# Kernel tuning notes

Measured on AMD Instinct MI355X. Metric: run time of the kernel, lower is better.

Reference implementation:

```python
import jax, jax.numpy as jnp
import numpy as np

C = 512
CQK = C // 8

def setup_inputs() -> dict:
    key = jax.random.key(0)
    ks = jax.random.split(key, 9)
    B, L = 8, 2048
    s = 0.02
    return {
        "x": jax.random.normal(ks[0], (B, C, L), jnp.float32),
        "Wq": jax.random.normal(ks[1], (CQK, C), jnp.float32) * s,
        "bq": jax.random.normal(ks[2], (CQK,), jnp.float32) * s,
        "Wk": jax.random.normal(ks[3], (CQK, C), jnp.float32) * s,
        "bk": jax.random.normal(ks[4], (CQK,), jnp.float32) * s,
        "Wv": jax.random.normal(ks[5], (C, C), jnp.float32) * s,
        "bv": jax.random.normal(ks[6], (C,), jnp.float32) * s,
        "Wo": jax.random.normal(ks[7], (C, C), jnp.float32) * s,
        "bo": jax.random.normal(ks[8], (C,), jnp.float32) * s,
    }

def reference(x, Wq, bq, Wk, bk, Wv, bv, Wo, bo):
    # x: [B, C, L]; 1x1 Conv1d == per-position linear over channels
    scale = CQK ** -0.5
    q = jnp.einsum('oc,bcl->bol', Wq, x) + bq[None, :, None]   # [B, CQK, L]
    k = jnp.einsum('oc,bcl->bol', Wk, x) + bk[None, :, None]   # [B, CQK, L]
    v = jnp.einsum('oc,bcl->bol', Wv, x) + bv[None, :, None]   # [B, C, L]
    scores = jnp.einsum('bcq,bck->bqk', q, k) * scale          # [B, L, L]
    attn = jax.nn.softmax(scores, axis=-1)
    out = jnp.einsum('bqk,bck->bcq', attn, v)                  # [B, C, L]
    out = jnp.einsum('oc,bcl->bol', Wo, out) + bo[None, :, None]
    return out + x
```

## Files before the change

kernel.cpp:

```cpp
#include <hip/hip_runtime.h>
#include <hip/hip_bf16.h>

typedef __hip_bfloat16 bf16;
using bf16x8 = __attribute__((ext_vector_type(8))) short;
using f32x4  = __attribute__((ext_vector_type(4))) float;

#define C_DIM 512
#define L_DIM 2048
#define B_DIM 8

#define MFMA16(a, b, c) __builtin_amdgcn_mfma_f32_16x16x32_bf16(a, b, c, 0, 0, 0)

__device__ __forceinline__ float fast_exp2(float x) {
#if __has_builtin(__builtin_amdgcn_exp2f)
    return __builtin_amdgcn_exp2f(x);
#else
    return exp2f(x);
#endif
}

static const size_t OFF_XT  = 0;
static const size_t OFF_WQB = 16777216;
static const size_t OFF_WKB = 16842752;
static const size_t OFF_WVB = 16908288;
static const size_t OFF_WOB = 17432576;
static const size_t OFF_QT  = 17956864;
static const size_t OFF_KT  = 20054016;
static const size_t OFF_VT  = 22151168;
static const size_t OFF_O1  = 38928384;

__global__ void k_wcvt(const float* __restrict__ Wq, const float* __restrict__ Wk,
                       const float* __restrict__ Wv, const float* __restrict__ Wo,
                       bf16* __restrict__ Wqb, bf16* __restrict__ Wkb,
                       bf16* __restrict__ Wvb, bf16* __restrict__ Wob) {
    int i = (blockIdx.x * 256 + threadIdx.x) * 2;
    const float* s;
    bf16* dst;
    if (i < 32768)       { s = Wq + i;            dst = Wqb + i; }
    else if (i < 65536)  { s = Wk + (i - 32768);  dst = Wkb + (i - 32768); }
    else if (i < 327680) { s = Wv + (i - 65536);  dst = Wvb + (i - 65536); }
    else                 { s = Wo + (i - 327680); dst = Wob + (i - 327680); }
    float2 v = *reinterpret_cast<const float2*>(s);
    *reinterpret_cast<__hip_bfloat162*>(dst) = __float22bfloat162_rn(make_float2(v.x, v.y));
}

__global__ __launch_bounds__(256) void k_tr(const float* __restrict__ x,
                                            bf16* __restrict__ xT) {
    __shared__ float T[64][65];
    const int b = blockIdx.z;
    const int l0 = blockIdx.x * 64, c0 = blockIdx.y * 64;
    const int tx = threadIdx.x & 63, ty = threadIdx.x >> 6;

    const float* xp = x + ((size_t)b * C_DIM + c0) * L_DIM + l0;
#pragma unroll
    for (int i = 0; i < 16; ++i) {
        int c = i * 4 + ty;
        T[c][tx] = xp[(size_t)c * L_DIM + tx];
    }
    __syncthreads();
    const int c2 = (threadIdx.x & 31) * 2;
    const int lr = threadIdx.x >> 5;
#pragma unroll
    for (int i = 0; i < 8; ++i) {
        int l = i * 8 + lr;
        __hip_bfloat162 u = __float22bfloat162_rn(make_float2(T[c2][l], T[c2 + 1][l]));
        *reinterpret_cast<__hip_bfloat162*>(
            &xT[((size_t)b * L_DIM + l0 + l) * C_DIM + c0 + c2]) = u;
    }
}

__global__ __launch_bounds__(256, 2) void k_qkv(const bf16* __restrict__ xT,
                                                const bf16* __restrict__ Wqb, const float* __restrict__ bq,
                                                const bf16* __restrict__ Wkb, const float* __restrict__ bk,
                                                const bf16* __restrict__ Wvb, const float* __restrict__ bv,
                                                bf16* __restrict__ qT, bf16* __restrict__ kT,
                                                bf16* __restrict__ vTT) {
    const int b = blockIdx.z, y = blockIdx.y, bx = blockIdx.x;
    const int tid = threadIdx.x;
    const int w = tid >> 6, lane = tid & 63, quad = lane >> 4, l15 = lane & 15;
    const int wm = w >> 1, wn = w & 1;
    const size_t bL = (size_t)b * L_DIM;

    __shared__ __align__(16) char lds[32768];

    const bf16* Aptr;
    const bf16* Bptr;
    if (y == 0) {
        Aptr = xT + (bL + bx * 128) * C_DIM;
        Bptr = Wqb;
    } else {
        Aptr = Wvb + (size_t)((y - 1) * 128) * C_DIM;
        Bptr = xT + (bL + bx * 128) * C_DIM;
    }

    f32x4 acc[4][4];
#pragma unroll
    for (int i = 0; i < 4; ++i)
#pragma unroll
        for (int j = 0; j < 4; ++j) acc[i][j] = (f32x4){0.f, 0.f, 0.f, 0.f};

    const int srow = tid >> 2;
    const int schk = tid & 3;
    auto stage = [&](int kt, int d) __attribute__((always_inline)) {
#pragma unroll
        for (int j = 0; j < 2; ++j) {
            const int row = j * 64 + srow;
            const int sg = schk ^ ((row >> 1) & 3);
            const bf16* sa = Aptr + (size_t)row * C_DIM + kt * 32 + sg * 8;
            __builtin_amdgcn_global_load_lds(
                (const __attribute__((address_space(1))) void*)sa,
                (__attribute__((address_space(3))) void*)(lds + d * 8192 + j * 4096 + w * 1024),
                16, 0, 0);
        }
#pragma unroll
        for (int j = 0; j < 2; ++j) {
            const int row = j * 64 + srow;
            const int sg = schk ^ ((row >> 1) & 3);
            const bf16* sb = Bptr + (size_t)row * C_DIM + kt * 32 + sg * 8;
            __builtin_amdgcn_global_load_lds(
                (const __attribute__((address_space(1))) void*)sb,
                (__attribute__((address_space(3))) void*)(lds + 16384 + d * 8192 + j * 4096 + w * 1024),
                16, 0, 0);
        }
    };

    const int fsw = (quad ^ ((l15 >> 1) & 3)) << 4;

    stage(0, 0);
    asm volatile("s_waitcnt vmcnt(0)" ::: "memory");
    __builtin_amdgcn_s_barrier();
    __builtin_amdgcn_sched_barrier(0);

    for (int kt = 0; kt < 16; ++kt) {
        const int d = kt & 1;
        if (kt < 15) stage(kt + 1, d ^ 1);

        char* Ab = lds + d * 8192;
        char* Bb = lds + 16384 + d * 8192;
        bf16x8 af[4], bfr[4];
#pragma unroll
        for (int mi = 0; mi < 4; ++mi)
            af[mi] = *(const bf16x8*)(Ab + (wm * 64 + mi * 16 + l15) * 64 + fsw);
#pragma unroll
        for (int ni = 0; ni < 4; ++ni)
            bfr[ni] = *(const bf16x8*)(Bb + (wn * 64 + ni * 16 + l15) * 64 + fsw);

#pragma unroll
        for (int mi = 0; mi < 4; ++mi)
#pragma unroll
            for (int ni = 0; ni < 4; ++ni)
                acc[mi][ni] = MFMA16(af[mi], bfr[ni], acc[mi][ni]);

        if (kt < 15) {
            asm volatile("s_waitcnt vmcnt(0)" ::: "memory");
            __builtin_amdgcn_s_barrier();
            __builtin_amdgcn_sched_barrier(0);
        }
    }

    if (y == 0) {
        const int mbase = bx * 128 + wm * 64;
        const float* bias = wn ? bk : bq;
        bf16* dst = wn ? kT : qT;
        const float sc = wn ? 1.0f : 0.18033688f;
        float bb[4];
#pragma unroll
        for (int ni = 0; ni < 4; ++ni) bb[ni] = bias[ni * 16 + l15];
#pragma unroll
        for (int mi = 0; mi < 4; ++mi)
#pragma unroll
            for (int r = 0; r < 4; ++r) {
                int l = mbase + mi * 16 + quad * 4 + r;
#pragma unroll
                for (int ni = 0; ni < 4; ++ni)
                    dst[(bL + l) * 64 + ni * 16 + l15] = __float2bfloat16((acc[mi][ni][r] + bb[ni]) * sc);
            }
    } else {
        const int cbase = (y - 1) * 128 + wm * 64;
        const int lbase = bx * 128 + wn * 64;
#pragma unroll
        for (int mi = 0; mi < 4; ++mi)
#pragma unroll
            for (int r = 0; r < 4; ++r) {
                int c = cbase + mi * 16 + quad * 4 + r;
                float bb = bv[c];
#pragma unroll
                for (int ni = 0; ni < 4; ++ni)
                    vTT[((size_t)b * C_DIM + c) * L_DIM + lbase + ni * 16 + l15] =
                        __float2bfloat16(acc[mi][ni][r] + bb);
            }
    }
}

__global__ __launch_bounds__(512, 4) void k_attn(const bf16* __restrict__ qT,
                                                 const bf16* __restrict__ kT,
                                                 const bf16* __restrict__ vTT,
                                                 bf16* __restrict__ o1) {
    const int bid = blockIdx.x;
    const int b  = bid & 7;
    const int qt = (bid >> 3) & 15;
    const int cs = bid >> 7;
    const int q0 = qt * 128;
    const int c0 = cs * 128;
    const int tid = threadIdx.x;
    const int w = tid >> 6, lane = tid & 63;
    const int quad = lane >> 4, l15 = lane & 15;

    __shared__ __align__(16) char lds[49152];

    const size_t bL = (size_t)b * L_DIM;
    const bf16* kb = kT + bL * 64;

    bf16x8 qf0, qf1;
    {
        const bf16* qrow = qT + (bL + q0 + w * 16 + l15) * 64;
        qf0 = *(const bf16x8*)(qrow + quad * 8);
        qf1 = *(const bf16x8*)(qrow + 32 + quad * 8);
    }

    f32x4 acc[8];
#pragma unroll
    for (int cg = 0; cg < 8; ++cg) acc[cg] = (f32x4){0.f, 0.f, 0.f, 0.f};
    f32x4 sacc = (f32x4){0.f, 0.f, 0.f, 0.f};

    bf16x8 onesB;
#pragma unroll
    for (int j = 0; j < 8; ++j) onesB[j] = (short)0x3F80;

    const int vbase = l15 * 64 + ((quad ^ ((l15 >> 1) & 3)) << 4);
    const int srcA  = ((quad & 1) * 32 + l15) * 4;

    auto stage = [&](int kt, int bufi) __attribute__((always_inline)) {
        {
            const int cl = tid >> 2, ps = tid & 3;
            const int pg = ps ^ ((cl >> 1) & 3);
            const bf16* src = vTT + ((size_t)b * C_DIM + c0 + cl) * L_DIM + kt * 32 + pg * 8;
            __builtin_amdgcn_global_load_lds(
                (const __attribute__((address_space(1))) void*)src,
                (__attribute__((address_space(3))) void*)(lds + bufi * 8192 + w * 1024),
                16, 0, 0);
        }
        {
            const int i = tid & 255, k = i >> 3, sl = i & 7;
            const int sg = sl ^ (k & 7);
            const bf16* src = kb + (size_t)(kt * 32 + k) * 64 + sg * 8;
            __builtin_amdgcn_global_load_lds(
                (const __attribute__((address_space(1))) void*)src,
                (__attribute__((address_space(3))) void*)(lds + 32768 + bufi * 4096 + (w & 3) * 1024),
                16, 0, 0);
        }
    };

    auto exppack = [&](const f32x4& s, unsigned& lo, unsigned& hi)
        __attribute__((always_inline)) {
        float p0 = fast_exp2(s[0] - 5.7707801f);
        float p1 = fast_exp2(s[1] - 5.7707801f);
        float p2 = fast_exp2(s[2] - 5.7707801f);
        float p3 = fast_exp2(s[3] - 5.7707801f);
        __hip_bfloat162 h01 = __float22bfloat162_rn(make_float2(p0, p1));
        __hip_bfloat162 h23 = __float22bfloat162_rn(make_float2(p2, p3));
        lo = *reinterpret_cast<unsigned*>(&h01);
        hi = *reinterpret_cast<unsigned*>(&h23);
    };

    bf16x8 paA, paB;

    auto step = [&](int i, bf16x8& paC, bf16x8& paN,
                    bool doPV, bool doStage, int vm) __attribute__((always_inline)) -> void {
        bf16x8 vBr[8];
        if (doPV) {
            char* Vb = lds + ((i - 1) & 3) * 8192;
#pragma unroll
            for (int cg = 0; cg < 8; ++cg)
                vBr[cg] = *(const bf16x8*)(Vb + vbase + cg * 1024);
        }
        if (vm == 0) asm volatile("s_waitcnt vmcnt(0)" ::: "memory");
        else         asm volatile("s_waitcnt vmcnt(2)" ::: "memory");
        __builtin_amdgcn_s_barrier();
        __builtin_amdgcn_sched_barrier(0);
        if (doStage) stage(i + 2, (i + 2) & 3);

        char* Kb = lds + 32768 + (i & 3) * 4096;
        bf16x8 kf[2][2];
#pragma unroll
        for (int kh = 0; kh < 2; ++kh)
#pragma unroll
            for (int h2 = 0; h2 < 2; ++h2)
                kf[kh][h2] = *(const bf16x8*)(Kb + (kh * 16 + l15) * 128 +
                                              (((h2 * 4 + quad) ^ (l15 & 7)) << 4));

        unsigned hh[2][2];
#pragma unroll
        for (int kh = 0; kh < 2; ++kh) {
            f32x4 s = {0.f, 0.f, 0.f, 0.f};
            s = MFMA16(kf[kh][0], qf0, s);
            s = MFMA16(kf[kh][1], qf1, s);
            exppack(s, hh[kh][0], hh[kh][1]);
        }

        if (doPV) {
#pragma unroll
            for (int cg = 0; cg < 8; ++cg)
                acc[cg] = MFMA16(paC, vBr[cg], acc[cg]);
            sacc = MFMA16(paC, onesB, sacc);
        }

        {
            int sel01 = (quad < 2) ? (int)hh[0][0] : (int)hh[1][0];
            int sel23 = (quad < 2) ? (int)hh[0][1] : (int)hh[1][1];
            int a0 = __builtin_amdgcn_ds_bpermute(srcA,      sel01);
            int a1 = __builtin_amdgcn_ds_bpermute(srcA,      sel23);
            int a2 = __builtin_amdgcn_ds_bpermute(srcA + 64, sel01);
            int a3 = __builtin_amdgcn_ds_bpermute(srcA + 64, sel23);
            int4 pi = make_int4(a0, a1, a2, a3);
            paN = *reinterpret_cast<bf16x8*>(&pi);
        }
    };

    stage(0, 0);
    stage(1, 1);
    step(0, paA, paA, false, true, 2);
    for (int i = 1; i < 63; i += 2) {
        step(i,     paA, paB, true, true,        2);
        step(i + 1, paB, paA, true, (i + 1) <= 61, 2);
    }
    step(63, paA, paB, true, false, 0);

    {
        char* Vb = lds + 3 * 8192;
#pragma unroll
        for (int cg = 0; cg < 8; ++cg) {
            bf16x8 vB = *(const bf16x8*)(Vb + vbase + cg * 1024);
            acc[cg] = MFMA16(paB, vB, acc[cg]);
        }
        sacc = MFMA16(paB, onesB, sacc);
    }

#pragma unroll
    for (int r = 0; r < 4; ++r) {
        float iv = 1.f / sacc[r];
        const size_t base = (bL + q0 + w * 16 + quad * 4 + r) * C_DIM + c0;
#pragma unroll
        for (int cg = 0; cg < 8; ++cg)
            o1[base + cg * 16 + l15] = __float2bfloat16(acc[cg][r] * iv);
    }
}

__global__ __launch_bounds__(256, 2) void k_out(const float* __restrict__ x,
                                                const bf16* __restrict__ Wob,
                                                const float* __restrict__ bo,
                                                const bf16* __restrict__ o1,
                                                float* __restrict__ out) {
    const int b = blockIdx.z;
    const int tid = threadIdx.x;
    const int w = tid >> 6, lane = tid & 63, quad = lane >> 4, l15 = lane & 15;
    const int wm = w >> 1, wn = w & 1;
    const int mbase = blockIdx.y * 128 + wm * 64;
    const int nbase = blockIdx.x * 128 + wn * 64;
    const size_t bL = (size_t)b * L_DIM;

    f32x4 acc[4][4];
#pragma unroll
    for (int i = 0; i < 4; ++i)
#pragma unroll
        for (int j = 0; j < 4; ++j) acc[i][j] = (f32x4){0.f, 0.f, 0.f, 0.f};

    const bf16* arow[4];
    const bf16* brow[4];
#pragma unroll
    for (int mi = 0; mi < 4; ++mi) arow[mi] = Wob + (size_t)(mbase + mi * 16 + l15) * C_DIM;
#pragma unroll
    for (int ni = 0; ni < 4; ++ni) brow[ni] = o1 + (bL + nbase + ni * 16 + l15) * C_DIM;

    bf16x8 af[4], bfr[4], afn[4], bfn[4];
    {
        const int ko = quad * 8;
#pragma unroll
        for (int mi = 0; mi < 4; ++mi) af[mi] = *(const bf16x8*)(arow[mi] + ko);
#pragma unroll
        for (int ni = 0; ni < 4; ++ni) bfr[ni] = *(const bf16x8*)(brow[ni] + ko);
    }
    for (int kt = 0; kt < 16; ++kt) {
        if (kt < 15) {
            const int ko = (kt + 1) * 32 + quad * 8;
#pragma unroll
            for (int mi = 0; mi < 4; ++mi) afn[mi] = *(const bf16x8*)(arow[mi] + ko);
#pragma unroll
            for (int ni = 0; ni < 4; ++ni) bfn[ni] = *(const bf16x8*)(brow[ni] + ko);
        }
#pragma unroll
        for (int mi = 0; mi < 4; ++mi)
#pragma unroll
            for (int ni = 0; ni < 4; ++ni)
                acc[mi][ni] = MFMA16(af[mi], bfr[ni], acc[mi][ni]);
#pragma unroll
        for (int i = 0; i < 4; ++i) { af[i] = afn[i]; bfr[i] = bfn[i]; }
    }

#pragma unroll
    for (int mi = 0; mi < 4; ++mi)
#pragma unroll
        for (int r = 0; r < 4; ++r) {
            int row = mbase + mi * 16 + quad * 4 + r;
            float bb = bo[row];
            size_t base = ((size_t)b * C_DIM + row) * L_DIM + nbase;
#pragma unroll
            for (int ni = 0; ni < 4; ++ni) {
                size_t idx = base + ni * 16 + l15;
                out[idx] = acc[mi][ni][r] + bb + x[idx];
            }
        }
}

extern "C" void kernel_launch(void* const* d_in, const int* in_sizes, int n_in,
                              void* d_out, int out_size, void* d_ws, size_t ws_size,
                              hipStream_t stream) {
    const float* x  = (const float*)d_in[0];
    const float* Wq = (const float*)d_in[1];
    const float* bq = (const float*)d_in[2];
    const float* Wk = (const float*)d_in[3];
    const float* bk = (const float*)d_in[4];
    const float* Wv = (const float*)d_in[5];
    const float* bv = (const float*)d_in[6];
    const float* Wo = (const float*)d_in[7];
    const float* bo = (const float*)d_in[8];

    char* wsb = (char*)d_ws;
    bf16* xT  = (bf16*)(wsb + OFF_XT);
    bf16* Wqb = (bf16*)(wsb + OFF_WQB);
    bf16* Wkb = (bf16*)(wsb + OFF_WKB);
    bf16* Wvb = (bf16*)(wsb + OFF_WVB);
    bf16* Wob = (bf16*)(wsb + OFF_WOB);
    bf16* qT  = (bf16*)(wsb + OFF_QT);
    bf16* kT  = (bf16*)(wsb + OFF_KT);
    bf16* vTT = (bf16*)(wsb + OFF_VT);
    bf16* o1  = (bf16*)(wsb + OFF_O1);
    float* out = (float*)d_out;

    k_wcvt<<<dim3(1152), 256, 0, stream>>>(Wq, Wk, Wv, Wo, Wqb, Wkb, Wvb, Wob);
    k_tr<<<dim3(L_DIM / 64, C_DIM / 64, B_DIM), 256, 0, stream>>>(x, xT);
    k_qkv<<<dim3(16, 5, B_DIM), 256, 0, stream>>>(xT, Wqb, bq, Wkb, bk, Wvb, bv, qT, kT, vTT);
    k_attn<<<dim3(512), 512, 0, stream>>>(qT, kT, vTT, o1);
    k_out<<<dim3(16, 4, B_DIM), 256, 0, stream>>>(x, Wob, bo, o1, out);
}
```

Baseline: 143.4 us.

## Stage k_out GEMM operands through swizzled LDS with direct global-to-LDS loads

```diff
diff --git a/kernel.cpp b/kernel.cpp
--- a/kernel.cpp
+++ b/kernel.cpp
@@ -355,48 +355,80 @@
     const int tid = threadIdx.x;
     const int w = tid >> 6, lane = tid & 63, quad = lane >> 4, l15 = lane & 15;
     const int wm = w >> 1, wn = w & 1;
+    const size_t bL = (size_t)b * L_DIM;
+
+    __shared__ __align__(16) char lds[32768];
+
+    const bf16* Aptr = Wob + (size_t)(blockIdx.y * 128) * C_DIM;
+    const bf16* Bptr = o1 + (bL + blockIdx.x * 128) * C_DIM;
+
+    f32x4 acc[4][4];
+#pragma unroll
+    for (int i = 0; i < 4; ++i)
+#pragma unroll
+        for (int j = 0; j < 4; ++j) acc[i][j] = (f32x4){0.f, 0.f, 0.f, 0.f};
+
+    const int srow = tid >> 2;
+    const int schk = tid & 3;
+    auto stage = [&](int kt, int d) __attribute__((always_inline)) {
+#pragma unroll
+        for (int j = 0; j < 2; ++j) {
+            const int row = j * 64 + srow;
+            const int sg = schk ^ ((row >> 1) & 3);
+            const bf16* sa = Aptr + (size_t)row * C_DIM + kt * 32 + sg * 8;
+            __builtin_amdgcn_global_load_lds(
+                (const __attribute__((address_space(1))) void*)sa,
+                (__attribute__((address_space(3))) void*)(lds + d * 8192 + j * 4096 + w * 1024),
+                16, 0, 0);
+        }
+#pragma unroll
+        for (int j = 0; j < 2; ++j) {
+            const int row = j * 64 + srow;
+            const int sg = schk ^ ((row >> 1) & 3);
+            const bf16* sb = Bptr + (size_t)row * C_DIM + kt * 32 + sg * 8;
+            __builtin_amdgcn_global_load_lds(
+                (const __attribute__((address_space(1))) void*)sb,
+                (__attribute__((address_space(3))) void*)(lds + 16384 + d * 8192 + j * 4096 + w * 1024),
+                16, 0, 0);
+        }
+    };
+
+    const int fsw = (quad ^ ((l15 >> 1) & 3)) << 4;
+
+    stage(0, 0);
+    asm volatile("s_waitcnt vmcnt(0)" ::: "memory");
+    __builtin_amdgcn_s_barrier();
+    __builtin_amdgcn_sched_barrier(0);
+
+    for (int kt = 0; kt < 16; ++kt) {
+        const int d = kt & 1;
+        if (kt < 15) stage(kt + 1, d ^ 1);
+
+        char* Ab = lds + d * 8192;
+        char* Bb = lds + 16384 + d * 8192;
+        bf16x8 af[4], bfr[4];
+#pragma unroll
+        for (int mi = 0; mi < 4; ++mi)
+            af[mi] = *(const bf16x8*)(Ab + (wm * 64 + mi * 16 + l15) * 64 + fsw);
+#pragma unroll
+        for (int ni = 0; ni < 4; ++ni)
+            bfr[ni] = *(const bf16x8*)(Bb + (wn * 64 + ni * 16 + l15) * 64 + fsw);
+
+#pragma unroll
+        for (int mi = 0; mi < 4; ++mi)
+#pragma unroll
+            for (int ni = 0; ni < 4; ++ni)
+                acc[mi][ni] = MFMA16(af[mi], bfr[ni], acc[mi][ni]);
+
+        if (kt < 15) {
+            asm volatile("s_waitcnt vmcnt(0)" ::: "memory");
+            __builtin_amdgcn_s_barrier();
+            __builtin_amdgcn_sched_barrier(0);
+        }
+    }
+
     const int mbase = blockIdx.y * 128 + wm * 64;
     const int nbase = blockIdx.x * 128 + wn * 64;
-    const size_t bL = (size_t)b * L_DIM;
-
-    f32x4 acc[4][4];
-#pragma unroll
-    for (int i = 0; i < 4; ++i)
-#pragma unroll
-        for (int j = 0; j < 4; ++j) acc[i][j] = (f32x4){0.f, 0.f, 0.f, 0.f};
-
-    const bf16* arow[4];
-    const bf16* brow[4];
-#pragma unroll
-    for (int mi = 0; mi < 4; ++mi) arow[mi] = Wob + (size_t)(mbase + mi * 16 + l15) * C_DIM;
-#pragma unroll
-    for (int ni = 0; ni < 4; ++ni) brow[ni] = o1 + (bL + nbase + ni * 16 + l15) * C_DIM;
-
-    bf16x8 af[4], bfr[4], afn[4], bfn[4];
-    {
-        const int ko = quad * 8;
-#pragma unroll
-        for (int mi = 0; mi < 4; ++mi) af[mi] = *(const bf16x8*)(arow[mi] + ko);
-#pragma unroll
-        for (int ni = 0; ni < 4; ++ni) bfr[ni] = *(const bf16x8*)(brow[ni] + ko);
-    }
-    for (int kt = 0; kt < 16; ++kt) {
-        if (kt < 15) {
-            const int ko = (kt + 1) * 32 + quad * 8;
-#pragma unroll
-            for (int mi = 0; mi < 4; ++mi) afn[mi] = *(const bf16x8*)(arow[mi] + ko);
-#pragma unroll
-            for (int ni = 0; ni < 4; ++ni) bfn[ni] = *(const bf16x8*)(brow[ni] + ko);
-        }
-#pragma unroll
-        for (int mi = 0; mi < 4; ++mi)
-#pragma unroll
-            for (int ni = 0; ni < 4; ++ni)
-                acc[mi][ni] = MFMA16(af[mi], bfr[ni], acc[mi][ni]);
-#pragma unroll
-        for (int i = 0; i < 4; ++i) { af[i] = afn[i]; bfr[i] = bfn[i]; }
-    }
-
 #pragma unroll
     for (int mi = 0; mi < 4; ++mi)
 #pragma unroll
```

Result: faster. 124.6 us (-13.1%).
